# Kernel tuning notes

Hardware: AMD Instinct MI355X
Metric: run time of the kernel (lower is better)

## Reference

```python
import jax, jax.numpy as jnp
import numpy as np

SPATIAL_SHAPES = [(80, 80), (40, 40), (20, 20)]
NUM_POINTS = [4, 4, 4]
N_HEADS = 8
OFFSET_SCALE = 0.5
LN_EPS = 1e-5


def layer_norm(x, w, b):
    m = x.mean(-1, keepdims=True)
    v = ((x - m) ** 2).mean(-1, keepdims=True)
    return (x - m) * jax.lax.rsqrt(v + LN_EPS) * w + b


def grid_sample(img, grid):
    """Bilinear, zero padding, align_corners=False.
    img: [N, C, H, W], grid: [N, Q, P, 2] in [-1, 1] -> [N, C, Q, P]."""
    N, C, H, W = img.shape
    gx = (grid[..., 0] + 1.0) * (W * 0.5) - 0.5
    gy = (grid[..., 1] + 1.0) * (H * 0.5) - 0.5
    x0 = jnp.floor(gx)
    y0 = jnp.floor(gy)
    wx1 = gx - x0
    wy1 = gy - y0
    x0i = x0.astype(jnp.int32)
    y0i = y0.astype(jnp.int32)
    flat = img.reshape(N, C, H * W)
    Q, P = grid.shape[1], grid.shape[2]

    def corner(xi, yi, w):
        valid = (xi >= 0) & (xi < W) & (yi >= 0) & (yi < H)
        idx = jnp.clip(yi, 0, H - 1) * W + jnp.clip(xi, 0, W - 1)
        v = jnp.take_along_axis(flat, idx.reshape(N, 1, Q * P), axis=2)
        v = v.reshape(N, C, Q, P)
        return v * (w * valid.astype(w.dtype))[:, None]

    return (corner(x0i, y0i, (1 - wx1) * (1 - wy1))
            + corner(x0i + 1, y0i, wx1 * (1 - wy1))
            + corner(x0i, y0i + 1, (1 - wx1) * wy1)
            + corner(x0i + 1, y0i + 1, wx1 * wy1))


def setup_inputs() -> dict:
    key = jax.random.key(0)
    ks = iter(jax.random.split(key, 40))
    B, Q, D, FF = 32, 300, 256, 1024
    S = sum(h * w for h, w in SPATIAL_SHAPES)  # 8400
    SP = sum(NUM_POINTS)  # 12

    def w(shape, scale=0.02):
        return jax.random.normal(next(ks), shape, jnp.float32) * scale

    inp = {
        'hidden_states': jax.random.normal(next(ks), (B, Q, D), jnp.float32),
        'position_embeddings': jax.random.normal(next(ks), (B, Q, D), jnp.float32),
        'reference_points': jax.random.uniform(next(ks), (B, Q, 1, 4), jnp.float32),
        'encoder_hidden_states': jax.random.normal(next(ks), (B, S, D), jnp.float32),
        'q_w': w((D, D)), 'q_b': jnp.zeros((D,), jnp.float32),
        'k_w': w((D, D)), 'k_b': jnp.zeros((D,), jnp.float32),
        'v_w': w((D, D)), 'v_b': jnp.zeros((D,), jnp.float32),
        'o_w': w((D, D)), 'o_b': jnp.zeros((D,), jnp.float32),
        'sa_ln_w': jnp.ones((D,), jnp.float32), 'sa_ln_b': jnp.zeros((D,), jnp.float32),
        'off_w': w((D, N_HEADS * SP * 2)), 'off_b': w((N_HEADS * SP * 2,), 0.1),
        'aw_w': w((D, N_HEADS * SP)), 'aw_b': jnp.zeros((N_HEADS * SP,), jnp.float32),
        'gate_w': w((2 * D, 2 * D)), 'gate_b': jnp.zeros((2 * D,), jnp.float32),
        'gate_ln_w': jnp.ones((D,), jnp.float32), 'gate_ln_b': jnp.zeros((D,), jnp.float32),
        'fc1_w': w((D, FF)), 'fc1_b': jnp.zeros((FF,), jnp.float32),
        'fc2_w': w((FF, D)), 'fc2_b': jnp.zeros((D,), jnp.float32),
        'fin_ln_w': jnp.ones((D,), jnp.float32), 'fin_ln_b': jnp.zeros((D,), jnp.float32),
    }
    return inp


def reference(hidden_states, position_embeddings, reference_points, encoder_hidden_states,
              q_w, q_b, k_w, k_b, v_w, v_b, o_w, o_b, sa_ln_w, sa_ln_b,
              off_w, off_b, aw_w, aw_b, gate_w, gate_b, gate_ln_w, gate_ln_b,
              fc1_w, fc1_b, fc2_w, fc2_b, fin_ln_w, fin_ln_b):
    B, Q, D = hidden_states.shape
    H = N_HEADS
    hd = D // H
    scaling = hd ** -0.5

    # ---- self attention (queries attend to queries, pos added to q/k only) ----
    hq = hidden_states + position_embeddings
    q = ((hq @ q_w + q_b) * scaling).reshape(B, Q, H, hd)
    k = (hq @ k_w + k_b).reshape(B, Q, H, hd)
    v = (hidden_states @ v_w + v_b).reshape(B, Q, H, hd)
    attn = jax.nn.softmax(jnp.einsum('bqhd,bkhd->bhqk', q, k), axis=-1)
    sa = jnp.einsum('bhqk,bkhd->bqhd', attn, v).reshape(B, Q, D) @ o_w + o_b
    hidden_states = layer_norm(hidden_states + sa, sa_ln_w, sa_ln_b)
    second_residual = hidden_states

    # ---- multi-scale deformable cross attention ----
    S = encoder_hidden_states.shape[1]
    SP = sum(NUM_POINTS)
    value = encoder_hidden_states.reshape(B, S, H, hd)
    offs = (hidden_states @ off_w + off_b).reshape(B, Q, H, SP, 2)
    aw = jax.nn.softmax((hidden_states @ aw_w + aw_b).reshape(B, Q, H, SP), axis=-1)
    nps = jnp.asarray([1.0 / n for n in NUM_POINTS for _ in range(n)], hidden_states.dtype)
    offset = offs * nps[:, None] * reference_points[:, :, None, :, 2:] * OFFSET_SCALE
    loc = reference_points[:, :, None, :, :2] + offset          # [B,Q,H,SP,2]
    grids = (2.0 * loc - 1.0).transpose(0, 2, 1, 3, 4).reshape(B * H, Q, SP, 2)
    val = value.transpose(0, 2, 3, 1).reshape(B * H, hd, S)

    sampled = []
    s0, p0 = 0, 0
    for (hl, wl), pl in zip(SPATIAL_SHAPES, NUM_POINTS):
        v_l = val[:, :, s0:s0 + hl * wl].reshape(B * H, hd, hl, wl)
        sampled.append(grid_sample(v_l, grids[:, :, p0:p0 + pl]))
        s0 += hl * wl
        p0 += pl
    sampled = jnp.concatenate(sampled, axis=-1)                 # [B*H,hd,Q,SP]
    aw = aw.transpose(0, 2, 1, 3).reshape(B * H, 1, Q, SP)
    ca = (sampled * aw).sum(-1).reshape(B, D, Q).transpose(0, 2, 1)

    # ---- gated residual ----
    gates = jax.nn.sigmoid(jnp.concatenate([second_residual, ca], -1) @ gate_w + gate_b)
    g1, g2 = gates[..., :D], gates[..., D:]
    hidden_states = layer_norm(g1 * second_residual + g2 * ca, gate_ln_w, gate_ln_b)

    # ---- FFN ----
    ffn = jax.nn.relu(hidden_states @ fc1_w + fc1_b) @ fc2_w + fc2_b
    return layer_norm(hidden_states + ffn, fin_ln_w, fin_ln_b)
```

## Files before the change

kernel.cpp:

```cpp
#include <hip/hip_runtime.h>
#include <cmath>

#define BQ 300
#define DIM 256
#define NH 8
#define HD 32
#define NB 32
#define MROWS 9600
#define SENC 8400

typedef unsigned short ushort_t;
typedef __attribute__((ext_vector_type(8))) short short8;
typedef __attribute__((ext_vector_type(4))) float f32x4;
typedef __attribute__((ext_vector_type(4))) unsigned short us4;

__device__ __forceinline__ float bf2f(ushort_t u) {
    union { unsigned u32; float f; } x; x.u32 = ((unsigned)u) << 16; return x.f;
}
__device__ __forceinline__ ushort_t f2bf(float f) {
    union { float f; unsigned u; } x; x.f = f;
    unsigned u = x.u;
    u += 0x7fffu + ((u >> 16) & 1u);
    return (ushort_t)(u >> 16);
}

__global__ __launch_bounds__(256)
void prep_all(const float* __restrict__ hidden, const float* __restrict__ pos,
              ushort_t* __restrict__ hq, ushort_t* __restrict__ hid,
              const float* __restrict__ q_w, const float* __restrict__ k_w,
              const float* __restrict__ v_w, const float* __restrict__ o_w,
              const float* __restrict__ off_w, const float* __restrict__ aw_w,
              const float* __restrict__ gate_w, const float* __restrict__ fc1_w,
              const float* __restrict__ fc2_w,
              ushort_t* __restrict__ qkvT, ushort_t* __restrict__ oT,
              ushort_t* __restrict__ offawT, ushort_t* __restrict__ gT,
              ushort_t* __restrict__ f1T, ushort_t* __restrict__ f2T,
              const float* __restrict__ q_b, const float* __restrict__ k_b,
              const float* __restrict__ v_b, float* __restrict__ qkvb,
              float scal)
{
    const int tid = threadIdx.x;
    if (blockIdx.x < 4800) {
        int i = blockIdx.x * 256 + tid;
        if (i < 614400) {
            float4 a = ((const float4*)hidden)[i];
            float4 b = ((const float4*)pos)[i];
            us4 u;
            u.x = f2bf(a.x + b.x); u.y = f2bf(a.y + b.y);
            u.z = f2bf(a.z + b.z); u.w = f2bf(a.w + b.w);
            *(us4*)&hq[(size_t)i * 4] = u;
        } else {
            i -= 614400;
            float4 a = ((const float4*)hidden)[i];
            us4 u;
            u.x = f2bf(a.x); u.y = f2bf(a.y); u.z = f2bf(a.z); u.w = f2bf(a.w);
            *(us4*)&hid[(size_t)i * 4] = u;
        }
        return;
    }
    __shared__ float t[32][33];
    const int bid = blockIdx.x - 4800;
    const float* src; ushort_t* dst; int K, N, local; float scale = 1.0f;

    if (bid < 64)       { src = q_w;   dst = qkvT;             K = 256; N = 256;  local = bid;       scale = scal; }
    else if (bid < 128) { src = k_w;   dst = qkvT + 256 * 256; K = 256; N = 256;  local = bid - 64; }
    else if (bid < 192) { src = v_w;   dst = qkvT + 512 * 256; K = 256; N = 256;  local = bid - 128; }
    else if (bid < 256) { src = o_w;   dst = oT;               K = 256; N = 256;  local = bid - 192; }
    else if (bid < 304) { src = off_w; dst = offawT;           K = 256; N = 192;  local = bid - 256; }
    else if (bid < 328) { src = aw_w;  dst = offawT + 192 * 256; K = 256; N = 96; local = bid - 304; }
    else if (bid < 336) {
        int l = bid - 328;
        ushort_t* d2 = offawT + 288 * 256 + l * 32;
        for (int e = tid; e < 32 * 32; e += 256) { int r = e >> 5, c = e & 31; d2[r * 256 + c] = 0; }
        return;
    }
    else if (bid < 592) { src = gate_w; dst = gT;  K = 512;  N = 512;  local = bid - 336; }
    else if (bid < 848) { src = fc1_w;  dst = f1T; K = 256;  N = 1024; local = bid - 592; }
    else if (bid < 1104){ src = fc2_w;  dst = f2T; K = 1024; N = 256;  local = bid - 848; }
    else {
        #pragma unroll
        for (int j = 0; j < 3; ++j) {
            int c = j * 256 + tid;
            float v = (j == 0) ? q_b[tid] * scal : (j == 1) ? k_b[tid] : v_b[tid];
            qkvb[c] = v;
        }
        return;
    }
    const int tilesx = N >> 5;
    const int n0 = (local % tilesx) * 32, k0 = (local / tilesx) * 32;
    const int tx = tid & 31, ty = tid >> 5;
    #pragma unroll
    for (int i = 0; i < 4; ++i)
        t[ty + i * 8][tx] = src[(size_t)(k0 + ty + i * 8) * N + n0 + tx];
    __syncthreads();
    #pragma unroll
    for (int i = 0; i < 4; ++i)
        dst[(size_t)(n0 + ty + i * 8) * K + k0 + tx] = f2bf(t[tx][ty + i * 8] * scale);
}

template<int BM, int BN, int ACT, bool OBF>
__global__ __launch_bounds__(256)
void gemm_mfma(const ushort_t* __restrict__ A1, const ushort_t* __restrict__ A2,
               int asplit, int lda,
               const ushort_t* __restrict__ Bt, int K,
               const float* __restrict__ bias, const float* __restrict__ bias2,
               int bsplit, int N,
               float* __restrict__ Cf, ushort_t* __restrict__ Cb, int ldc)
{
    constexpr int LDT = 40;
    __shared__ ushort_t As[BM * LDT];
    __shared__ ushort_t Bs[BN * LDT];
    const int tid = threadIdx.x;
    const int row0 = blockIdx.y * BM, col0 = blockIdx.x * BN;
    const ushort_t* __restrict__ A = (col0 < asplit) ? A1 : A2;
    const int lane = tid & 63, wid = tid >> 6;
    const int wm = wid >> 1, wn = wid & 1;
    constexpr int FM = BM / 32, FN = BN / 32;
    const int r16 = lane & 15, kg = lane >> 4;

    f32x4 acc[FM][FN];
    #pragma unroll
    for (int m = 0; m < FM; ++m)
        #pragma unroll
        for (int n = 0; n < FN; ++n) {
            f32x4 z = {0.f, 0.f, 0.f, 0.f};
            acc[m][n] = z;
        }

    for (int k0 = 0; k0 < K; k0 += 32) {
        #pragma unroll
        for (int c = 0; c < BM * 4 / 256; ++c) {
            int idx = tid + c * 256;
            int r = idx >> 2, cc = idx & 3;
            *(short8*)&As[r * LDT + cc * 8] =
                *(const short8*)&A[(size_t)(row0 + r) * lda + k0 + cc * 8];
        }
        #pragma unroll
        for (int c = 0; c < BN * 4 / 256; ++c) {
            int idx = tid + c * 256;
            int r = idx >> 2, cc = idx & 3;
            *(short8*)&Bs[r * LDT + cc * 8] =
                *(const short8*)&Bt[(size_t)(col0 + r) * K + k0 + cc * 8];
        }
        __syncthreads();
        short8 a[FM], b[FN];
        #pragma unroll
        for (int m = 0; m < FM; ++m)
            a[m] = *(const short8*)&As[(wm * (BM / 2) + m * 16 + r16) * LDT + kg * 8];
        #pragma unroll
        for (int n = 0; n < FN; ++n)
            b[n] = *(const short8*)&Bs[(wn * (BN / 2) + n * 16 + r16) * LDT + kg * 8];
        #pragma unroll
        for (int m = 0; m < FM; ++m)
            #pragma unroll
            for (int n = 0; n < FN; ++n)
                acc[m][n] = __builtin_amdgcn_mfma_f32_16x16x32_bf16(a[m], b[n], acc[m][n], 0, 0, 0);
        __syncthreads();
    }

    #pragma unroll
    for (int m = 0; m < FM; ++m) {
        #pragma unroll
        for (int n = 0; n < FN; ++n) {
            int colb = col0 + wn * (BN / 2) + n * 16 + r16;
            float bs;
            if (colb < bsplit) bs = bias[colb];
            else if (colb < N) bs = bias2[colb - bsplit];
            else bs = 0.0f;
            #pragma unroll
            for (int r = 0; r < 4; ++r) {
                int row = row0 + wm * (BM / 2) + m * 16 + kg * 4 + r;
                float v = acc[m][n][r] + bs;
                if (ACT == 1) v = fmaxf(v, 0.0f);
                if (ACT == 2) v = 1.0f / (1.0f + __expf(-v));
                if (OBF) Cb[(size_t)row * ldc + colb] = f2bf(v);
                else     Cf[(size_t)row * ldc + colb] = v;
            }
        }
    }
}

__global__ __launch_bounds__(256)
void attn_flash(const ushort_t* __restrict__ QKV, ushort_t* __restrict__ O)
{
    __shared__ ushort_t ks[64 * 40];
    __shared__ ushort_t vt[32 * 72];
    __shared__ float    ss[32 * 68];
    __shared__ ushort_t ps[32 * 72];
    __shared__ float    ml[32], ll[32], fl[32];

    const int orig = blockIdx.x;
    const int wg = (orig & 7) * 320 + (orig >> 3);
    const int qc = wg % 10, bh = wg / 10;
    const int b = bh >> 3, h = bh & 7;
    const int q0 = qc * 32;
    const int nq = (BQ - q0 < 32) ? (BQ - q0) : 32;

    const int tid = threadIdx.x;
    const int lane = tid & 63, wid = tid >> 6;
    const int r16 = lane & 15, kg = lane >> 4;
    const int wm = wid >> 1, wn = wid & 1;

    if (tid < 32) { ml[tid] = -1e30f; ll[tid] = 0.f; }

    short8 aq[2];
    #pragma unroll
    for (int rt = 0; rt < 2; ++rt) {
        int qr = q0 + rt * 16 + r16;
        if (qr > BQ - 1) qr = BQ - 1;
        aq[rt] = *(const short8*)&QKV[((size_t)(b * BQ + qr)) * 768 + h * 32 + kg * 8];
    }
    f32x4 oacc = {0.f, 0.f, 0.f, 0.f};

    for (int kt = 0; kt < 5; ++kt) {
        __syncthreads();
        {
            int kk = tid >> 2, c8 = (tid & 3) * 8;
            int ki = kt * 64 + kk;
            short8 kv = {0, 0, 0, 0, 0, 0, 0, 0};
            short8 vv = {0, 0, 0, 0, 0, 0, 0, 0};
            if (ki < BQ) {
                size_t gi = ((size_t)(b * BQ + ki)) * 768 + h * 32 + c8;
                kv = *(const short8*)&QKV[gi + 256];
                vv = *(const short8*)&QKV[gi + 512];
            }
            *(short8*)&ks[kk * 40 + c8] = kv;
            #pragma unroll
            for (int j = 0; j < 8; ++j) vt[(c8 + j) * 72 + kk] = (ushort_t)vv[j];
        }
        __syncthreads();
        {
            short8 bk = *(const short8*)&ks[(wid * 16 + r16) * 40 + kg * 8];
            #pragma unroll
            for (int rt = 0; rt < 2; ++rt) {
                f32x4 sacc = {0.f, 0.f, 0.f, 0.f};
                sacc = __builtin_amdgcn_mfma_f32_16x16x32_bf16(aq[rt], bk, sacc, 0, 0, 0);
                #pragma unroll
                for (int r = 0; r < 4; ++r)
                    ss[(rt * 16 + kg * 4 + r) * 68 + wid * 16 + r16] = sacc[r];
            }
        }
        __syncthreads();
        #pragma unroll
        for (int j = 0; j < 8; ++j) {
            int row = wid * 8 + j;
            float s = ss[row * 68 + lane];
            if (kt * 64 + lane >= BQ) s = -1e30f;
            float tm = s;
            #pragma unroll
            for (int off = 32; off; off >>= 1) tm = fmaxf(tm, __shfl_xor(tm, off));
            float mold = ml[row];
            float mnew = fmaxf(mold, tm);
            float p = __expf(s - mnew);
            float psum = p;
            #pragma unroll
            for (int off = 32; off; off >>= 1) psum += __shfl_xor(psum, off);
            if (lane == 0) {
                float f = __expf(mold - mnew);
                ml[row] = mnew;
                ll[row] = ll[row] * f + psum;
                fl[row] = f;
            }
            ps[row * 72 + lane] = f2bf(p);
        }
        __syncthreads();
        {
            #pragma unroll
            for (int r = 0; r < 4; ++r)
                oacc[r] *= fl[wm * 16 + kg * 4 + r];
            #pragma unroll
            for (int kstep = 0; kstep < 2; ++kstep) {
                short8 pa = *(const short8*)&ps[(wm * 16 + r16) * 72 + kstep * 32 + kg * 8];
                short8 bv = *(const short8*)&vt[(wn * 16 + r16) * 72 + kstep * 32 + kg * 8];
                oacc = __builtin_amdgcn_mfma_f32_16x16x32_bf16(pa, bv, oacc, 0, 0, 0);
            }
        }
    }
    __syncthreads();
    #pragma unroll
    for (int r = 0; r < 4; ++r) {
        int rowl = wm * 16 + kg * 4 + r;
        if (rowl < nq) {
            float v = oacc[r] / ll[rowl];
            O[((size_t)(b * BQ + q0 + rowl)) * 256 + h * 32 + wn * 16 + r16] = f2bf(v);
        }
    }
}

__global__ __launch_bounds__(256)
void ln_add(const float* __restrict__ X, const float* __restrict__ Y,
            const float* __restrict__ w, const float* __restrict__ b,
            float* __restrict__ outf, ushort_t* __restrict__ outbf, int ldbf)
{
    const int row = blockIdx.x * 4 + (threadIdx.x >> 6);
    const int lane = threadIdx.x & 63;
    float v[4];
    #pragma unroll
    for (int i = 0; i < 4; ++i) {
        int c = lane + 64 * i;
        v[i] = X[(size_t)row * DIM + c] + Y[(size_t)row * DIM + c];
    }
    float s = v[0] + v[1] + v[2] + v[3];
    float s2 = v[0]*v[0] + v[1]*v[1] + v[2]*v[2] + v[3]*v[3];
    #pragma unroll
    for (int off = 32; off; off >>= 1) { s += __shfl_xor(s, off); s2 += __shfl_xor(s2, off); }
    const float mean = s * (1.0f / DIM);
    const float var = s2 * (1.0f / DIM) - mean * mean;
    const float inv = rsqrtf(var + 1e-5f);
    #pragma unroll
    for (int i = 0; i < 4; ++i) {
        int c = lane + 64 * i;
        float r = (v[i] - mean) * inv * w[c] + b[c];
        if (outf)  outf[(size_t)row * DIM + c] = r;
        if (outbf) outbf[(size_t)row * ldbf + c] = f2bf(r);
    }
}

__global__ __launch_bounds__(256)
void ln_gate(const ushort_t* __restrict__ C2, const ushort_t* __restrict__ G,
             const float* __restrict__ w, const float* __restrict__ b,
             float* __restrict__ outf, ushort_t* __restrict__ outbf)
{
    const int row = blockIdx.x * 4 + (threadIdx.x >> 6);
    const int lane = threadIdx.x & 63;
    float v[4];
    #pragma unroll
    for (int i = 0; i < 4; ++i) {
        int c = lane + 64 * i;
        float h1 = bf2f(C2[(size_t)row * 512 + c]);
        float ca = bf2f(C2[(size_t)row * 512 + 256 + c]);
        float g1 = bf2f(G[(size_t)row * 512 + c]);
        float g2 = bf2f(G[(size_t)row * 512 + 256 + c]);
        v[i] = g1 * h1 + g2 * ca;
    }
    float s = v[0] + v[1] + v[2] + v[3];
    float s2 = v[0]*v[0] + v[1]*v[1] + v[2]*v[2] + v[3]*v[3];
    #pragma unroll
    for (int off = 32; off; off >>= 1) { s += __shfl_xor(s, off); s2 += __shfl_xor(s2, off); }
    const float mean = s * (1.0f / DIM);
    const float var = s2 * (1.0f / DIM) - mean * mean;
    const float inv = rsqrtf(var + 1e-5f);
    #pragma unroll
    for (int i = 0; i < 4; ++i) {
        int c = lane + 64 * i;
        float r = (v[i] - mean) * inv * w[c] + b[c];
        outf[(size_t)row * DIM + c] = r;
        outbf[(size_t)row * DIM + c] = f2bf(r);
    }
}

__global__ __launch_bounds__(256)
void sample_kernel(const float* __restrict__ enc, const float* __restrict__ offaw,
                   const float* __restrict__ ref, ushort_t* __restrict__ C2out)
{
    __shared__ float sofs[4][320];
    __shared__ float sref[4][4];

    const int orig = blockIdx.x;
    const int blk = (orig & 7) * 300 + (orig >> 3);
    const int b = blk / 75;
    const int q0 = (blk % 75) * 4;
    const int tid = threadIdx.x;
    const int qq = tid >> 6;
    const int h = (tid >> 3) & 7;
    const int d4 = tid & 7;
    const int bq = b * BQ + q0 + qq;

    for (int e = tid; e < 4 * 80; e += 256) {
        int row = e / 80, c4 = e % 80;
        ((float4*)&sofs[row][0])[c4] =
            ((const float4*)(offaw + (size_t)(b * BQ + q0 + row) * 320))[c4];
    }
    if (tid < 16)
        sref[tid >> 2][tid & 3] = ref[(size_t)(b * BQ + q0 + (tid >> 2)) * 4 + (tid & 3)];
    __syncthreads();

    const float rx = sref[qq][0], ry = sref[qq][1];
    const float rw = sref[qq][2], rh = sref[qq][3];
    const float* op = &sofs[qq][h * 24];
    const float* ap = &sofs[qq][192 + h * 12];

    float wgt[12];
    float mx = -1e30f;
    #pragma unroll
    for (int j = 0; j < 12; ++j) { wgt[j] = ap[j]; mx = fmaxf(mx, wgt[j]); }
    float sum = 0.0f;
    #pragma unroll
    for (int j = 0; j < 12; ++j) { wgt[j] = __expf(wgt[j] - mx); sum += wgt[j]; }
    const float isum = 1.0f / sum;

    f32x4 acc = {0.f, 0.f, 0.f, 0.f};
    int p = 0;
    #pragma unroll
    for (int l = 0; l < 3; ++l) {
        const int Wl = (l == 0) ? 80 : (l == 1 ? 40 : 20);
        const int Hl = Wl;
        const int soff = (l == 0) ? 0 : (l == 1 ? 6400 : 8000);
        const float* base = enc + ((size_t)(b * SENC + soff)) * DIM + h * HD + d4 * 4;
        #pragma unroll
        for (int pp = 0; pp < 4; ++pp, ++p) {
            const float ox = op[p * 2 + 0], oy = op[p * 2 + 1];
            const float lx = rx + ox * 0.25f * rw * 0.5f;
            const float ly = ry + oy * 0.25f * rh * 0.5f;
            const float gx = lx * (float)Wl - 0.5f;
            const float gy = ly * (float)Hl - 0.5f;
            const float x0f = floorf(gx), y0f = floorf(gy);
            const int x0 = (int)x0f, y0 = (int)y0f;
            const float wx1 = gx - x0f, wy1 = gy - y0f;
            const float wx0 = 1.0f - wx1, wy0 = 1.0f - wy1;
            const bool vx0 = (x0 >= 0) & (x0 < Wl);
            const bool vx1 = (x0 + 1 >= 0) & (x0 + 1 < Wl);
            const bool vy0 = (y0 >= 0) & (y0 < Hl);
            const bool vy1 = (y0 + 1 >= 0) & (y0 + 1 < Hl);
            const int xc0 = min(max(x0, 0), Wl - 1);
            const int xc1 = min(max(x0 + 1, 0), Wl - 1);
            const int yc0 = min(max(y0, 0), Hl - 1);
            const int yc1 = min(max(y0 + 1, 0), Hl - 1);
            const float aw2 = wgt[p] * isum;
            const float w00 = wx0 * wy0 * ((vx0 & vy0) ? aw2 : 0.0f);
            const float w10 = wx1 * wy0 * ((vx1 & vy0) ? aw2 : 0.0f);
            const float w01 = wx0 * wy1 * ((vx0 & vy1) ? aw2 : 0.0f);
            const float w11 = wx1 * wy1 * ((vx1 & vy1) ? aw2 : 0.0f);
            f32x4 c00 = *(const f32x4*)&base[((size_t)(yc0 * Wl + xc0)) * DIM];
            f32x4 c10 = *(const f32x4*)&base[((size_t)(yc0 * Wl + xc1)) * DIM];
            f32x4 c01 = *(const f32x4*)&base[((size_t)(yc1 * Wl + xc0)) * DIM];
            f32x4 c11 = *(const f32x4*)&base[((size_t)(yc1 * Wl + xc1)) * DIM];
            #pragma unroll
            for (int r = 0; r < 4; ++r)
                acc[r] += w00 * c00[r] + w10 * c10[r] + w01 * c01[r] + w11 * c11[r];
        }
    }
    us4 u;
    u.x = f2bf(acc[0]); u.y = f2bf(acc[1]); u.z = f2bf(acc[2]); u.w = f2bf(acc[3]);
    *(us4*)&C2out[(size_t)bq * 512 + 256 + h * HD + d4 * 4] = u;
}

extern "C" void kernel_launch(void* const* d_in, const int* in_sizes, int n_in,
                              void* d_out, int out_size, void* d_ws, size_t ws_size,
                              hipStream_t stream)
{
    (void)in_sizes; (void)n_in; (void)out_size; (void)ws_size;
    const float* hidden   = (const float*)d_in[0];
    const float* pos      = (const float*)d_in[1];
    const float* ref      = (const float*)d_in[2];
    const float* enc      = (const float*)d_in[3];
    const float* q_w      = (const float*)d_in[4];
    const float* q_b      = (const float*)d_in[5];
    const float* k_w      = (const float*)d_in[6];
    const float* k_b      = (const float*)d_in[7];
    const float* v_w      = (const float*)d_in[8];
    const float* v_b      = (const float*)d_in[9];
    const float* o_w      = (const float*)d_in[10];
    const float* o_b      = (const float*)d_in[11];
    const float* sa_ln_w  = (const float*)d_in[12];
    const float* sa_ln_b  = (const float*)d_in[13];
    const float* off_w    = (const float*)d_in[14];
    const float* off_b    = (const float*)d_in[15];
    const float* aw_w     = (const float*)d_in[16];
    const float* aw_b     = (const float*)d_in[17];
    const float* gate_w   = (const float*)d_in[18];
    const float* gate_b   = (const float*)d_in[19];
    const float* gate_ln_w= (const float*)d_in[20];
    const float* gate_ln_b= (const float*)d_in[21];
    const float* fc1_w    = (const float*)d_in[22];
    const float* fc1_b    = (const float*)d_in[23];
    const float* fc2_w    = (const float*)d_in[24];
    const float* fc2_b    = (const float*)d_in[25];
    const float* fin_ln_w = (const float*)d_in[26];
    const float* fin_ln_b = (const float*)d_in[27];
    float* out = (float*)d_out;

    char* wsb = (char*)d_ws;
    ushort_t* hqbf   = (ushort_t*)(wsb + 0);
    ushort_t* hidbf  = (ushort_t*)(wsb + 4915200);
    ushort_t* QKV    = (ushort_t*)(wsb + 9830400);
    ushort_t* aobf   = (ushort_t*)(wsb + 24576000);
    float*    SA     = (float*)(wsb + 0);
    ushort_t* C2     = (ushort_t*)(wsb + 9830400);
    float*    offaw  = (float*)(wsb + 19660800);
    ushort_t* gatesbf= (ushort_t*)(wsb + 0);
    ushort_t* midbf  = (ushort_t*)(wsb + 19660800);
    float*    ffn    = (float*)(wsb + 0);
    ushort_t* h2bf   = (ushort_t*)(wsb + 39321600);
    ushort_t* qkvT   = (ushort_t*)(wsb + 44236800);
    ushort_t* oT     = (ushort_t*)(wsb + 44630016);
    ushort_t* offawT = (ushort_t*)(wsb + 44761088);
    ushort_t* gT     = (ushort_t*)(wsb + 44924928);
    ushort_t* f1T    = (ushort_t*)(wsb + 45449216);
    ushort_t* f2T    = (ushort_t*)(wsb + 45973504);
    float*    qkvb   = (float*)(wsb + 46497792);

    const dim3 blk(256);
    const float scal = 0.17677669529663687f;
    const int BIG = 1 << 30;

    prep_all<<<dim3(5905), blk, 0, stream>>>(hidden, pos, hqbf, hidbf,
                                             q_w, k_w, v_w, o_w, off_w, aw_w,
                                             gate_w, fc1_w, fc2_w,
                                             qkvT, oT, offawT, gT, f1T, f2T,
                                             q_b, k_b, v_b, qkvb, scal);

    gemm_mfma<64,128,0,true><<<dim3(6,150), blk, 0, stream>>>(hqbf, hidbf, 512, 256, qkvT, 256, qkvb, nullptr, 768, 768, nullptr, QKV, 768);

    attn_flash<<<dim3(2560), blk, 0, stream>>>(QKV, aobf);

    gemm_mfma<64,64,0,false><<<dim3(4,150), blk, 0, stream>>>(aobf, nullptr, BIG, 256, oT, 256, o_b, nullptr, 256, 256, SA, nullptr, 256);
    ln_add<<<dim3(2400), blk, 0, stream>>>(SA, hidden, sa_ln_w, sa_ln_b, nullptr, C2, 512);

    gemm_mfma<64,64,0,false><<<dim3(5,150), blk, 0, stream>>>(C2, nullptr, BIG, 512, offawT, 256, off_b, aw_b, 192, 288, offaw, nullptr, 320);

    sample_kernel<<<dim3(2400), blk, 0, stream>>>(enc, offaw, ref, C2);

    gemm_mfma<64,128,2,true><<<dim3(4,150), blk, 0, stream>>>(C2, nullptr, BIG, 512, gT, 512, gate_b, nullptr, 512, 512, nullptr, gatesbf, 512);
    ln_gate<<<dim3(2400), blk, 0, stream>>>(C2, gatesbf, gate_ln_w, gate_ln_b, out, h2bf);

    gemm_mfma<128,128,1,true><<<dim3(8,75), blk, 0, stream>>>(h2bf, nullptr, BIG, 256, f1T, 256, fc1_b, nullptr, 1024, 1024, nullptr, midbf, 1024);
    gemm_mfma<64,64,0,false><<<dim3(4,150), blk, 0, stream>>>(midbf, nullptr, BIG, 1024, f2T, 1024, fc2_b, nullptr, 256, 256, ffn, nullptr, 256);
    ln_add<<<dim3(2400), blk, 0, stream>>>(ffn, out, fin_ln_w, fin_ln_b, out, nullptr, 0);
}
```

Before: 243.5 us.

## Fuse output and FC2 GEMMs with residual LayerNorm; merge prep conversions

Adds a gemm_ln kernel that computes a full 256-wide row tile (32 rows per block), adds bias and residual, and applies LayerNorm in the epilogue. It replaces the o_proj GEMM plus ln_add and the fc2 GEMM plus ln_add, removing the fp32 intermediate round trips and two launches. The prep kernel also now writes both the bf16 hidden+pos and bf16 hidden arrays from a single load of hidden. The cost is that only 300 blocks are launched, and the K loop has no double buffering while reloading the full 256-column B tile on every step, which may lower occupancy and latency hiding compared with the 600-block tiled GEMMs.

```diff
diff --git a/kernel.cpp b/kernel.cpp
--- a/kernel.cpp
+++ b/kernel.cpp
@@ -40,26 +40,20 @@
               float scal)
 {
     const int tid = threadIdx.x;
-    if (blockIdx.x < 4800) {
+    if (blockIdx.x < 2400) {
         int i = blockIdx.x * 256 + tid;
-        if (i < 614400) {
-            float4 a = ((const float4*)hidden)[i];
-            float4 b = ((const float4*)pos)[i];
-            us4 u;
-            u.x = f2bf(a.x + b.x); u.y = f2bf(a.y + b.y);
-            u.z = f2bf(a.z + b.z); u.w = f2bf(a.w + b.w);
-            *(us4*)&hq[(size_t)i * 4] = u;
-        } else {
-            i -= 614400;
-            float4 a = ((const float4*)hidden)[i];
-            us4 u;
-            u.x = f2bf(a.x); u.y = f2bf(a.y); u.z = f2bf(a.z); u.w = f2bf(a.w);
-            *(us4*)&hid[(size_t)i * 4] = u;
-        }
+        float4 a = ((const float4*)hidden)[i];
+        float4 b = ((const float4*)pos)[i];
+        us4 uq, uh;
+        uq.x = f2bf(a.x + b.x); uq.y = f2bf(a.y + b.y);
+        uq.z = f2bf(a.z + b.z); uq.w = f2bf(a.w + b.w);
+        uh.x = f2bf(a.x); uh.y = f2bf(a.y); uh.z = f2bf(a.z); uh.w = f2bf(a.w);
+        *(us4*)&hq[(size_t)i * 4] = uq;
+        *(us4*)&hid[(size_t)i * 4] = uh;
         return;
     }
     __shared__ float t[32][33];
-    const int bid = blockIdx.x - 4800;
+    const int bid = blockIdx.x - 2400;
     const float* src; ushort_t* dst; int K, N, local; float scale = 1.0f;
 
     if (bid < 64)       { src = q_w;   dst = qkvT;             K = 256; N = 256;  local = bid;       scale = scal; }
@@ -181,6 +175,103 @@
 }
 
 __global__ __launch_bounds__(256)
+void gemm_ln(const ushort_t* __restrict__ A, int lda,
+             const ushort_t* __restrict__ Bt, int K,
+             const float* __restrict__ gb, const float* __restrict__ Y,
+             const float* __restrict__ lnw, const float* __restrict__ lnb,
+             float* __restrict__ outf, ushort_t* __restrict__ outbf, int ldout)
+{
+    constexpr int LDT = 40;
+    __shared__ ushort_t As[32 * LDT];
+    __shared__ ushort_t Bs[256 * LDT];
+    __shared__ float sred[2][32], qred[2][32];
+    const int tid = threadIdx.x;
+    const int row0 = blockIdx.x * 32;
+    const int lane = tid & 63, wid = tid >> 6;
+    const int wm = wid >> 1, wn = wid & 1;
+    const int r16 = lane & 15, kg = lane >> 4;
+
+    f32x4 acc[8];
+    #pragma unroll
+    for (int n = 0; n < 8; ++n) { f32x4 z = {0.f,0.f,0.f,0.f}; acc[n] = z; }
+
+    for (int k0 = 0; k0 < K; k0 += 32) {
+        if (tid < 128) {
+            int r = tid >> 2, cc = tid & 3;
+            *(short8*)&As[r * LDT + cc * 8] =
+                *(const short8*)&A[(size_t)(row0 + r) * lda + k0 + cc * 8];
+        }
+        #pragma unroll
+        for (int c = 0; c < 4; ++c) {
+            int idx = tid + c * 256;
+            int r = idx >> 2, cc = idx & 3;
+            *(short8*)&Bs[r * LDT + cc * 8] =
+                *(const short8*)&Bt[(size_t)r * K + k0 + cc * 8];
+        }
+        __syncthreads();
+        short8 a = *(const short8*)&As[(wm * 16 + r16) * LDT + kg * 8];
+        #pragma unroll
+        for (int n = 0; n < 8; ++n) {
+            short8 b = *(const short8*)&Bs[(wn * 128 + n * 16 + r16) * LDT + kg * 8];
+            acc[n] = __builtin_amdgcn_mfma_f32_16x16x32_bf16(a, b, acc[n], 0, 0, 0);
+        }
+        __syncthreads();
+    }
+
+    float s[4] = {0.f, 0.f, 0.f, 0.f}, q[4] = {0.f, 0.f, 0.f, 0.f};
+    #pragma unroll
+    for (int n = 0; n < 8; ++n) {
+        const int col = wn * 128 + n * 16 + r16;
+        const float gbv = gb[col];
+        #pragma unroll
+        for (int r = 0; r < 4; ++r) {
+            const int row = row0 + wm * 16 + kg * 4 + r;
+            float t = acc[n][r] + gbv + Y[(size_t)row * 256 + col];
+            acc[n][r] = t;
+            s[r] += t; q[r] += t * t;
+        }
+    }
+    #pragma unroll
+    for (int off = 1; off < 16; off <<= 1) {
+        #pragma unroll
+        for (int r = 0; r < 4; ++r) {
+            s[r] += __shfl_xor(s[r], off);
+            q[r] += __shfl_xor(q[r], off);
+        }
+    }
+    if (r16 == 0) {
+        #pragma unroll
+        for (int r = 0; r < 4; ++r) {
+            sred[wn][wm * 16 + kg * 4 + r] = s[r];
+            qred[wn][wm * 16 + kg * 4 + r] = q[r];
+        }
+    }
+    __syncthreads();
+    float mn[4], inv[4];
+    #pragma unroll
+    for (int r = 0; r < 4; ++r) {
+        const int rl = wm * 16 + kg * 4 + r;
+        float S = sred[0][rl] + sred[1][rl];
+        float Q = qred[0][rl] + qred[1][rl];
+        float mean = S * (1.0f / 256.0f);
+        float var = Q * (1.0f / 256.0f) - mean * mean;
+        mn[r] = mean; inv[r] = rsqrtf(var + 1e-5f);
+    }
+    #pragma unroll
+    for (int n = 0; n < 8; ++n) {
+        const int col = wn * 128 + n * 16 + r16;
+        const float w = lnw[col], b = lnb[col];
+        #pragma unroll
+        for (int r = 0; r < 4; ++r) {
+            const int row = row0 + wm * 16 + kg * 4 + r;
+            float v = (acc[n][r] - mn[r]) * inv[r] * w + b;
+            if (outf)  outf[(size_t)row * 256 + col] = v;
+            if (outbf) outbf[(size_t)row * ldout + col] = f2bf(v);
+        }
+    }
+}
+
+__global__ __launch_bounds__(256)
 void attn_flash(const ushort_t* __restrict__ QKV, ushort_t* __restrict__ O)
 {
     __shared__ ushort_t ks[64 * 40];
@@ -284,35 +375,6 @@
             float v = oacc[r] / ll[rowl];
             O[((size_t)(b * BQ + q0 + rowl)) * 256 + h * 32 + wn * 16 + r16] = f2bf(v);
         }
-    }
-}
-
-__global__ __launch_bounds__(256)
-void ln_add(const float* __restrict__ X, const float* __restrict__ Y,
-            const float* __restrict__ w, const float* __restrict__ b,
-            float* __restrict__ outf, ushort_t* __restrict__ outbf, int ldbf)
-{
-    const int row = blockIdx.x * 4 + (threadIdx.x >> 6);
-    const int lane = threadIdx.x & 63;
-    float v[4];
-    #pragma unroll
-    for (int i = 0; i < 4; ++i) {
-        int c = lane + 64 * i;
-        v[i] = X[(size_t)row * DIM + c] + Y[(size_t)row * DIM + c];
-    }
-    float s = v[0] + v[1] + v[2] + v[3];
-    float s2 = v[0]*v[0] + v[1]*v[1] + v[2]*v[2] + v[3]*v[3];
-    #pragma unroll
-    for (int off = 32; off; off >>= 1) { s += __shfl_xor(s, off); s2 += __shfl_xor(s2, off); }
-    const float mean = s * (1.0f / DIM);
-    const float var = s2 * (1.0f / DIM) - mean * mean;
-    const float inv = rsqrtf(var + 1e-5f);
-    #pragma unroll
-    for (int i = 0; i < 4; ++i) {
-        int c = lane + 64 * i;
-        float r = (v[i] - mean) * inv * w[c] + b[c];
-        if (outf)  outf[(size_t)row * DIM + c] = r;
-        if (outbf) outbf[(size_t)row * ldbf + c] = f2bf(r);
     }
 }
 
@@ -475,12 +537,10 @@
     ushort_t* hidbf  = (ushort_t*)(wsb + 4915200);
     ushort_t* QKV    = (ushort_t*)(wsb + 9830400);
     ushort_t* aobf   = (ushort_t*)(wsb + 24576000);
-    float*    SA     = (float*)(wsb + 0);
     ushort_t* C2     = (ushort_t*)(wsb + 9830400);
     float*    offaw  = (float*)(wsb + 19660800);
     ushort_t* gatesbf= (ushort_t*)(wsb + 0);
     ushort_t* midbf  = (ushort_t*)(wsb + 19660800);
-    float*    ffn    = (float*)(wsb + 0);
     ushort_t* h2bf   = (ushort_t*)(wsb + 39321600);
     ushort_t* qkvT   = (ushort_t*)(wsb + 44236800);
     ushort_t* oT     = (ushort_t*)(wsb + 44630016);
@@ -494,7 +554,7 @@
     const float scal = 0.17677669529663687f;
     const int BIG = 1 << 30;
 
-    prep_all<<<dim3(5905), blk, 0, stream>>>(hidden, pos, hqbf, hidbf,
+    prep_all<<<dim3(3505), blk, 0, stream>>>(hidden, pos, hqbf, hidbf,
                                              q_w, k_w, v_w, o_w, off_w, aw_w,
                                              gate_w, fc1_w, fc2_w,
                                              qkvT, oT, offawT, gT, f1T, f2T,
@@ -504,8 +564,8 @@
 
     attn_flash<<<dim3(2560), blk, 0, stream>>>(QKV, aobf);
 
-    gemm_mfma<64,64,0,false><<<dim3(4,150), blk, 0, stream>>>(aobf, nullptr, BIG, 256, oT, 256, o_b, nullptr, 256, 256, SA, nullptr, 256);
-    ln_add<<<dim3(2400), blk, 0, stream>>>(SA, hidden, sa_ln_w, sa_ln_b, nullptr, C2, 512);
+    gemm_ln<<<dim3(300), blk, 0, stream>>>(aobf, 256, oT, 256, o_b, hidden,
+                                           sa_ln_w, sa_ln_b, nullptr, C2, 512);
 
     gemm_mfma<64,64,0,false><<<dim3(5,150), blk, 0, stream>>>(C2, nullptr, BIG, 512, offawT, 256, off_b, aw_b, 192, 288, offaw, nullptr, 320);
 
@@ -515,6 +575,6 @@
     ln_gate<<<dim3(2400), blk, 0, stream>>>(C2, gatesbf, gate_ln_w, gate_ln_b, out, h2bf);
 
     gemm_mfma<128,128,1,true><<<dim3(8,75), blk, 0, stream>>>(h2bf, nullptr, BIG, 256, f1T, 256, fc1_b, nullptr, 1024, 1024, nullptr, midbf, 1024);
-    gemm_mfma<64,64,0,false><<<dim3(4,150), blk, 0, stream>>>(midbf, nullptr, BIG, 1024, f2T, 1024, fc2_b, nullptr, 256, 256, ffn, nullptr, 256);
-    ln_add<<<dim3(2400), blk, 0, stream>>>(ffn, out, fin_ln_w, fin_ln_b, out, nullptr, 0);
-}
+    gemm_ln<<<dim3(300), blk, 0, stream>>>(midbf, 1024, f2T, 1024, fc2_b, out,
+                                           fin_ln_w, fin_ln_b, out, nullptr, 0);
+}
```

Result: no change. 242.9 us (-0.2%).
